# Kernel tuning notes

Hardware: AMD Instinct MI355X
Metric: run time of the kernel (lower is better)

Reference implementation:

```python
import jax, jax.numpy as jnp
import numpy as np

NUM_COMPONENTS = 4
HEADS = 16


def setup_inputs() -> dict:
    key = jax.random.key(0)
    ks = jax.random.split(key, 7)
    BC, S, D = 8, 4096, 1024      # batch_times_comp = batch(2) * num_components(4)
    Se, De = 256, 2048            # encoder seq len, encoder hidden dim
    sc = 0.02                     # keep linear outputs in a sane range
    return {
        "hidden_states": jax.random.normal(ks[0], (BC, S, D), jnp.float32),
        "encoder_hidden_states": jax.random.normal(ks[1], (BC, Se, De), jnp.float32),
        "Wq": jax.random.normal(ks[2], (D, D), jnp.float32) * sc,
        "Wk": jax.random.normal(ks[3], (De, D), jnp.float32) * sc,
        "Wv": jax.random.normal(ks[4], (De, D), jnp.float32) * sc,
        "Wo": jax.random.normal(ks[5], (D, D), jnp.float32) * sc,
        "bo": jnp.zeros((D,), jnp.float32),
    }


def reference(hidden_states, encoder_hidden_states, Wq, Wk, Wv, Wo, bo):
    C, H = NUM_COMPONENTS, HEADS
    BC, S, D = hidden_states.shape
    Se = encoder_hidden_states.shape[1]
    B = BC // C
    dh = D // H
    scale = dh ** -0.5  # attn.scale (learn_temperature=False)

    # projections -> [BC, H, S(e), dh]
    q = (hidden_states @ Wq).reshape(BC, S, H, dh).transpose(0, 2, 1, 3)
    k = (encoder_hidden_states @ Wk).reshape(BC, Se, H, dh).transpose(0, 2, 1, 3)
    v = (encoder_hidden_states @ Wv).reshape(BC, Se, H, dh).transpose(0, 2, 1, 3)

    # dense scores [BC, H, S, Se]
    scores = jnp.einsum("bhsd,bhtd->bhst", q, k) * scale
    # softmax over the COMPONENT axis (dim 0 after the 5D view)
    scores5 = scores.reshape(C, B, H, S, Se)
    w = jax.nn.softmax(scores5, axis=0)  # [C, B, H, S, Se]

    # compositional (negative) entropy, summed over components -> [B, H, S, Se]
    compositional_entropy = (w * jnp.log(w)).sum(axis=0)

    # rescale and attend
    w = (w * (C / Se)).reshape(BC, H, S, Se)
    out = jnp.einsum("bhst,bhtd->bhsd", w, v)
    out = out.transpose(0, 2, 1, 3).reshape(BC, S, D)

    # to_out[0] linear (+bias), to_out[1] dropout = identity at eval,
    # residual connection, rescale_output_factor = 1
    out = out @ Wo + bo + hidden_states
    return out, compositional_entropy
```

## Files before the change

### kernel.cpp

```cpp
#include <hip/hip_runtime.h>

typedef unsigned short u16;
typedef __bf16 bf16x4 __attribute__((ext_vector_type(4)));
typedef __bf16 bf16x8 __attribute__((ext_vector_type(8)));
typedef float f32x4 __attribute__((ext_vector_type(4)));
typedef u16 u16x4 __attribute__((ext_vector_type(4)));
typedef u16 u16x8 __attribute__((ext_vector_type(8)));

#define AS1P(p) ((__attribute__((address_space(1))) void*)(unsigned long long)(p))
#define AS3P(p) ((__attribute__((address_space(3))) void*)(unsigned long long)(p))
#define MFMA16(a, b, c) __builtin_amdgcn_mfma_f32_16x16x32_bf16((a), (b), (c), 0, 0, 0)

__device__ __forceinline__ u16 f2b(float x) { return __builtin_bit_cast(u16, (__bf16)x); }
__device__ __forceinline__ float b2f(u16 u) {
  return __builtin_bit_cast(float, (unsigned)u << 16);
}

__global__ __launch_bounds__(256) void cvt_f32_bf16(const float* __restrict__ in,
                                                    u16* __restrict__ out, int n4) {
  int stride = gridDim.x * blockDim.x;
  for (int i = blockIdx.x * blockDim.x + threadIdx.x; i < n4; i += stride) {
    f32x4 v = *(const f32x4*)(in + (long)i * 4);
    u16x4 o;
    o[0] = f2b(v[0]); o[1] = f2b(v[1]); o[2] = f2b(v[2]); o[3] = f2b(v[3]);
    *(u16x4*)(out + (long)i * 4) = o;
  }
}

__global__ __launch_bounds__(256) void wtrans(const float* __restrict__ W,
                                              u16* __restrict__ Wt, int K, int N) {
  __shared__ float tile[32][33];
  int nbk = K >> 5;
  int bk = blockIdx.x % nbk;
  int bn = blockIdx.x / nbk;
  int tx = threadIdx.x & 31, ty = threadIdx.x >> 5;
#pragma unroll
  for (int i = 0; i < 32; i += 8)
    tile[ty + i][tx] = W[(long)(bk * 32 + ty + i) * N + bn * 32 + tx];
  __syncthreads();
#pragma unroll
  for (int i = 0; i < 32; i += 8)
    Wt[(long)(bn * 32 + ty + i) * K + bk * 32 + tx] = f2b(tile[tx][ty + i]);
}

__global__ __launch_bounds__(256) void vtrans(const u16* __restrict__ kvb,
                                              u16* __restrict__ vt) {
  __shared__ u16 tile[32][33];
  int bt = blockIdx.x & 7;
  int bd = (blockIdx.x >> 3) & 31;
  int bc = blockIdx.x >> 8;
  int tx = threadIdx.x & 31, ty = threadIdx.x >> 5;
  const long ob = (long)bc * 1024 * 256;
  const float RS = 1.0f / 64.0f;
#pragma unroll
  for (int i = 0; i < 32; i += 8)
    tile[ty + i][tx] =
        kvb[((long)bc * 256 + bt * 32 + ty + i) * 2048 + 1024 + bd * 32 + tx];
  __syncthreads();
#pragma unroll
  for (int i = 0; i < 32; i += 8)
    vt[ob + (long)(bd * 32 + ty + i) * 256 + bt * 32 + tx] =
        f2b(b2f(tile[tx][ty + i]) * RS);
}

__global__ __launch_bounds__(256) void kfrag_build(const u16* __restrict__ kvb,
                                                   u16* __restrict__ kfrag) {
  int wv = ((int)blockIdx.x << 2) + (threadIdx.x >> 6);
  int lane = threadIdx.x & 63, lr = lane & 15, lg = lane >> 4;
  int ks = wv & 1, tsl = (wv >> 1) & 1, c = (wv >> 2) & 3;
  int ch = (wv >> 4) & 7, h = (wv >> 7) & 15, b = (wv >> 11) & 1;
  const u16* src = kvb + ((long)(c * 2 + b) * 256 + ch * 32 + tsl * 16 + lr) * 2048 +
                   h * 64 + ks * 32 + lg * 8;
  *(bf16x8*)(kfrag + (long)wv * 512 + lane * 8) = *(const bf16x8*)src;
}

__global__ __launch_bounds__(256) void vfrag_build(const u16* __restrict__ vtb,
                                                   u16* __restrict__ vfrag) {
  int wv = ((int)blockIdx.x << 2) + (threadIdx.x >> 6);
  int lane = threadIdx.x & 63, lr = lane & 15, lg = lane >> 4;
  int dsu = wv & 3, c = (wv >> 2) & 3;
  int ch = (wv >> 4) & 7, h = (wv >> 7) & 15, b = (wv >> 11) & 1;
  const u16* src = vtb + ((long)(c * 2 + b) * 1024 + h * 64 + dsu * 16 + lr) * 256 +
                   ch * 32 + lg * 8;
  *(bf16x8*)(vfrag + (long)wv * 512 + lane * 8) = *(const bf16x8*)src;
}

__global__ __launch_bounds__(256) void gemm_bt(
    const u16* __restrict__ A, const u16* __restrict__ Bt,
    u16* __restrict__ outb, int M, int N, int K, float ascale) {
  __shared__ u16 lA[128 * 64];
  __shared__ u16 lB[128 * 64];
  const int tid = threadIdx.x;
  const int lane = tid & 63;
  const int wid = tid >> 6;
  const int wm = wid >> 1, wn = wid & 1;
  const int lr = lane & 15, lg = lane >> 4;

  int bid = (int)blockIdx.x;
  int nwg = (int)gridDim.x;
  if ((nwg & 7) == 0) bid = (bid & 7) * (nwg >> 3) + (bid >> 3);

  const int nbn = N >> 7;
  const int bm = bid / nbn;
  const int bn = bid % nbn;
  const long arow0 = (long)bm * 128;
  const long brow0 = (long)bn * 128;

  f32x4 acc[4][4] = {};

  const int srow = tid >> 3;
  const int scol = tid & 7;

  for (int k0 = 0; k0 < K; k0 += 64) {
#pragma unroll
    for (int i = 0; i < 4; ++i) {
      int row = i * 32 + srow;
      int kc = scol ^ (row & 7);
      __builtin_amdgcn_global_load_lds(AS1P(A + (arow0 + row) * K + k0 + kc * 8),
                                       AS3P(lA + i * 2048 + (tid & ~63) * 8), 16, 0, 0);
    }
#pragma unroll
    for (int i = 0; i < 4; ++i) {
      int row = i * 32 + srow;
      int kc = scol ^ (row & 7);
      __builtin_amdgcn_global_load_lds(AS1P(Bt + (brow0 + row) * K + k0 + kc * 8),
                                       AS3P(lB + i * 2048 + (tid & ~63) * 8), 16, 0, 0);
    }
    asm volatile("s_waitcnt vmcnt(0)" ::: "memory");
    __syncthreads();

#pragma unroll
    for (int ks = 0; ks < 2; ++ks) {
      bf16x8 af[4], bfr[4];
#pragma unroll
      for (int m = 0; m < 4; ++m) {
        int row = wm * 64 + m * 16 + lr;
        int off = row * 128 + ks * 64 + lg * 16;
        off ^= (row & 7) << 4;
        af[m] = *(const bf16x8*)((const char*)lA + off);
      }
#pragma unroll
      for (int n = 0; n < 4; ++n) {
        int row = wn * 64 + n * 16 + lr;
        int off = row * 128 + ks * 64 + lg * 16;
        off ^= (row & 7) << 4;
        bfr[n] = *(const bf16x8*)((const char*)lB + off);
      }
#pragma unroll
      for (int m = 0; m < 4; ++m)
#pragma unroll
        for (int n = 0; n < 4; ++n)
          acc[m][n] = MFMA16(af[m], bfr[n], acc[m][n]);
    }
    __syncthreads();
  }

#pragma unroll
  for (int m = 0; m < 4; ++m)
#pragma unroll
    for (int n = 0; n < 4; ++n) {
      long col = brow0 + wn * 64 + n * 16 + lr;
#pragma unroll
      for (int r = 0; r < 4; ++r) {
        long row = arow0 + wm * 64 + m * 16 + lg * 4 + r;
        outb[row * N + col] = f2b(acc[m][n][r] * ascale);
      }
    }
}

template <int MODE>
__global__ __launch_bounds__(512, 2) void gemm256(
    const u16* __restrict__ A, const u16* __restrict__ Bt,
    u16* __restrict__ outb, float* __restrict__ outf,
    const float* __restrict__ bias, const u16* __restrict__ residb,
    int M, int N, int K, float ascale) {
  __shared__ u16 lds[2][2][256 * 64];
  const int tid = threadIdx.x;
  const int lane = tid & 63;
  const int wid = tid >> 6;
  const int wm = wid >> 2;
  const int wn = wid & 3;
  const int lr = lane & 15, lg = lane >> 4;

  int bid = (int)blockIdx.x;
  int nwg = (int)gridDim.x;
  bid = (bid & 7) * (nwg >> 3) + (bid >> 3);

  const int nbn = N >> 8;
  const int bm = bid / nbn;
  const int bn = bid % nbn;
  const long arow0 = (long)bm * 256;
  const long brow0 = (long)bn * 256;

  f32x4 acc[8][4] = {};

  const int srow = tid >> 3;
  const int scol = tid & 7;
  const int nt = K >> 6;

#define STAGE256(bf, t)                                                                \
  do {                                                                                 \
    int k0_ = (t) << 6;                                                                \
    _Pragma("unroll") for (int i = 0; i < 4; ++i) {                                    \
      int row = i * 64 + srow;                                                         \
      int kc = scol ^ (row & 7);                                                       \
      __builtin_amdgcn_global_load_lds(AS1P(A + (arow0 + row) * K + k0_ + kc * 8),     \
                                       AS3P(&lds[bf][0][0] + i * 4096 + (tid & ~63) * 8), \
                                       16, 0, 0);                                      \
    }                                                                                  \
    _Pragma("unroll") for (int i = 0; i < 4; ++i) {                                    \
      int row = i * 64 + srow;                                                         \
      int kc = scol ^ (row & 7);                                                       \
      __builtin_amdgcn_global_load_lds(AS1P(Bt + (brow0 + row) * K + k0_ + kc * 8),    \
                                       AS3P(&lds[bf][1][0] + i * 4096 + (tid & ~63) * 8), \
                                       16, 0, 0);                                      \
    }                                                                                  \
  } while (0)

#define COMPUTE256(bf)                                                                 \
  do {                                                                                 \
    _Pragma("unroll") for (int ks = 0; ks < 2; ++ks) {                                 \
      bf16x8 af[8], bfr[4];                                                            \
      _Pragma("unroll") for (int m = 0; m < 8; ++m) {                                  \
        int row = wm * 128 + m * 16 + lr;                                              \
        int off = row * 128 + ks * 64 + lg * 16;                                       \
        off ^= (row & 7) << 4;                                                         \
        af[m] = *(const bf16x8*)((const char*)&lds[bf][0][0] + off);                   \
      }                                                                                \
      _Pragma("unroll") for (int n = 0; n < 4; ++n) {                                  \
        int row = wn * 64 + n * 16 + lr;                                               \
        int off = row * 128 + ks * 64 + lg * 16;                                       \
        off ^= (row & 7) << 4;                                                         \
        bfr[n] = *(const bf16x8*)((const char*)&lds[bf][1][0] + off);                  \
      }                                                                                \
      _Pragma("unroll") for (int m = 0; m < 8; ++m)                                    \
          _Pragma("unroll") for (int n = 0; n < 4; ++n)                                \
              acc[m][n] = MFMA16(af[m], bfr[n], acc[m][n]);                            \
    }                                                                                  \
  } while (0)

  STAGE256(0, 0);
  asm volatile("s_waitcnt vmcnt(0)" ::: "memory");
  __syncthreads();
  int cur = 0;
  for (int t = 0; t < nt - 1; ++t) {
    STAGE256(cur ^ 1, t + 1);
    COMPUTE256(cur);
    asm volatile("s_waitcnt vmcnt(0)" ::: "memory");
    __syncthreads();
    cur ^= 1;
  }
  COMPUTE256(cur);

#pragma unroll
  for (int m = 0; m < 8; ++m)
#pragma unroll
    for (int n = 0; n < 4; ++n) {
      long col = brow0 + wn * 64 + n * 16 + lr;
#pragma unroll
      for (int r = 0; r < 4; ++r) {
        long row = arow0 + wm * 128 + m * 16 + lg * 4 + r;
        float v = acc[m][n][r];
        if (MODE == 1) {
          long idx = row * N + col;
          __builtin_nontemporal_store(v + bias[col] + b2f(residb[idx]), outf + idx);
        } else {
          outb[row * N + col] = f2b(v * ascale);
        }
      }
    }
#undef STAGE256
#undef COMPUTE256
}

__global__ __launch_bounds__(256, 1) void attn_fused(
    const u16* q,
    const u16* __restrict__ kfrag,
    const u16* __restrict__ vfrag,
    u16* attnout,
    float* __restrict__ ent) {
  const int B = 2, H = 16, S = 4096, Se = 256, D = 1024;
  __shared__ u16 kvs[2][32 * 512];
  __shared__ u16 ldsP[4 * 4608];
  const int tid = threadIdx.x;
  const int lane = tid & 63, wid = tid >> 6;
  const int lr = lane & 15, lg = lane >> 4;
  int bid = (int)blockIdx.x;
  bid = (bid & 7) * 128 + (bid >> 3);
  const int sblk = bid & 31;
  const int h = (bid >> 5) & 15;
  const int b = bid >> 9;
  const int s0 = sblk * 128 + wid * 32;

  u16* Pw = ldsP + wid * 4608;

  bf16x8 qf[4][2][2];
#pragma unroll
  for (int c = 0; c < 4; ++c)
#pragma unroll
    for (int st = 0; st < 2; ++st)
#pragma unroll
      for (int ks = 0; ks < 2; ++ks)
        qf[c][st][ks] =
            *(const bf16x8*)(q + ((c * B + b) * (long)S + s0 + st * 16 + lr) * D +
                             h * 64 + ks * 32 + lg * 8);

  const u16* kbh = kfrag + (long)(b * 16 + h) * 65536;
  const u16* vbh = vfrag + (long)(b * 16 + h) * 65536;
  float* entp = ent + ((long)(b * H + h) * S + s0 + lg * 4) * Se + lr;

  const float LN2 = 0.69314718056f;
  const int g0 = wid * 8;

  f32x4 oacc[4][4][2] = {};

#define STAGEKV(buf, ch)                                                               \
  do {                                                                                 \
    _Pragma("unroll") for (int j = 0; j < 8; ++j) {                                    \
      int f = g0 + j;                                                                  \
      const u16* src = (f < 16 ? kbh + (ch) * 8192 + f * 512                           \
                               : vbh + (ch) * 8192 + (f - 16) * 512) +                 \
                       lane * 8;                                                       \
      __builtin_amdgcn_global_load_lds(AS1P(src), AS3P(&kvs[buf][f * 512]), 16, 0, 0); \
    }                                                                                  \
  } while (0)

  STAGEKV(0, 0);
  __syncthreads();

#pragma unroll
  for (int ch = 0; ch < 8; ++ch) {
    const int cur = ch & 1;
    if (ch < 7) STAGEKV(cur ^ 1, ch + 1);
    const u16* KV = kvs[cur];

    f32x4 sacc[2][4][2] = {};
#pragma unroll
    for (int c = 0; c < 4; ++c)
#pragma unroll
      for (int tsl = 0; tsl < 2; ++tsl)
#pragma unroll
        for (int ks = 0; ks < 2; ++ks) {
          bf16x8 kfv = *(const bf16x8*)(KV + (c * 4 + tsl * 2 + ks) * 512 + lane * 8);
#pragma unroll
          for (int st = 0; st < 2; ++st)
            sacc[st][c][tsl] = MFMA16(qf[c][st][ks], kfv, sacc[st][c][tsl]);
        }

#pragma unroll
    for (int st = 0; st < 2; ++st) {
#pragma unroll
      for (int tsl = 0; tsl < 2; ++tsl) {
#pragma unroll
        for (int r = 0; r < 4; ++r) {
          float t0 = sacc[st][0][tsl][r];
          float t1 = sacc[st][1][tsl][r];
          float t2 = sacc[st][2][tsl][r];
          float t3 = sacc[st][3][tsl][r];
          float e0 = __builtin_amdgcn_exp2f(t0);
          float e1 = __builtin_amdgcn_exp2f(t1);
          float e2 = __builtin_amdgcn_exp2f(t2);
          float e3 = __builtin_amdgcn_exp2f(t3);
          float sum = (e0 + e1) + (e2 + e3);
          float inv = __builtin_amdgcn_rcpf(sum);
          float l2s = __builtin_amdgcn_logf(sum);
          float w0 = e0 * inv, w1 = e1 * inv, w2 = e2 * inv, w3 = e3 * inv;
          float entv = (w0 * t0 + w1 * t1 + w2 * t2 + w3 * t3 - l2s) * LN2;
          __builtin_nontemporal_store(
              entv, entp + (st * 16 + r) * Se + ch * 32 + tsl * 16);
          int prow = st * 16 + lg * 4 + r;
          int pof = prow * 36 + tsl * 16 + lr;
          Pw[0 * 1152 + pof] = f2b(w0);
          Pw[1 * 1152 + pof] = f2b(w1);
          Pw[2 * 1152 + pof] = f2b(w2);
          Pw[3 * 1152 + pof] = f2b(w3);
        }
      }
    }

#pragma unroll
    for (int c = 0; c < 4; ++c) {
      bf16x8 pf[2];
#pragma unroll
      for (int st = 0; st < 2; ++st) {
        union { bf16x4 hh[2]; bf16x8 v; } pu;
        pu.hh[0] = *(const bf16x4*)(Pw + c * 1152 + (st * 16 + lr) * 36 + lg * 8);
        pu.hh[1] = *(const bf16x4*)(Pw + c * 1152 + (st * 16 + lr) * 36 + lg * 8 + 4);
        pf[st] = pu.v;
      }
#pragma unroll
      for (int dsu = 0; dsu < 4; ++dsu) {
        bf16x8 vfv = *(const bf16x8*)(KV + (16 + c * 4 + dsu) * 512 + lane * 8);
        oacc[c][dsu][0] = MFMA16(pf[0], vfv, oacc[c][dsu][0]);
        oacc[c][dsu][1] = MFMA16(pf[1], vfv, oacc[c][dsu][1]);
      }
    }

    __syncthreads();
  }

#pragma unroll
  for (int c = 0; c < 4; ++c)
#pragma unroll
    for (int dsu = 0; dsu < 4; ++dsu)
#pragma unroll
      for (int st = 0; st < 2; ++st)
#pragma unroll
        for (int r = 0; r < 4; ++r) {
          long s = s0 + st * 16 + lg * 4 + r;
          attnout[((c * B + b) * (long)S + s) * D + h * 64 + dsu * 16 + lr] =
              f2b(oacc[c][dsu][st][r]);
        }
#undef STAGEKV
}

extern "C" void kernel_launch(void* const* d_in, const int* in_sizes, int n_in,
                              void* d_out, int out_size, void* d_ws, size_t ws_size,
                              hipStream_t stream) {
  const float* hs  = (const float*)d_in[0];
  const float* ehs = (const float*)d_in[1];
  const float* Wq  = (const float*)d_in[2];
  const float* Wk  = (const float*)d_in[3];
  const float* Wv  = (const float*)d_in[4];
  const float* Wo  = (const float*)d_in[5];
  const float* bo  = (const float*)d_in[6];
  float* out = (float*)d_out;
  float* ent = out + (size_t)8 * 4096 * 1024;

  char* ws = (char*)d_ws;
  u16* hsb   = (u16*)(ws);
  u16* ehsb  = (u16*)(ws + 67108864);
  u16* kfrag = (u16*)(ws + 67108864);
  u16* vfrag = (u16*)(ws + 71303168);
  u16* wqT   = (u16*)(ws + 75497472);
  u16* wkT   = (u16*)(ws + 77594624);
  u16* wvT   = (u16*)(ws + 81788928);
  u16* woT   = (u16*)(ws + 85983232);
  u16* qb    = (u16*)(ws + 88080384);
  u16* kvb   = (u16*)(ws + 155189248);
  u16* vtb   = (u16*)(ws + 163577856);

  const float QSCALE = 0.125f * 1.44269504f;

  cvt_f32_bf16<<<2048, 256, 0, stream>>>(hs, hsb, (8 * 4096 * 1024) / 4);
  cvt_f32_bf16<<<512, 256, 0, stream>>>(ehs, ehsb, (8 * 256 * 2048) / 4);
  wtrans<<<1024, 256, 0, stream>>>(Wq, wqT, 1024, 1024);
  wtrans<<<2048, 256, 0, stream>>>(Wk, wkT, 2048, 1024);
  wtrans<<<2048, 256, 0, stream>>>(Wv, wvT, 2048, 1024);
  wtrans<<<1024, 256, 0, stream>>>(Wo, woT, 1024, 1024);
  gemm256<0><<<(32768 / 256) * (1024 / 256), 512, 0, stream>>>(
      hsb, wqT, qb, nullptr, nullptr, nullptr, 32768, 1024, 1024, QSCALE);
  gemm_bt<<<(2048 / 128) * (2048 / 128), 256, 0, stream>>>(
      ehsb, wkT, kvb, 2048, 2048, 2048, 1.0f);
  vtrans<<<2048, 256, 0, stream>>>(kvb, vtb);
  kfrag_build<<<1024, 256, 0, stream>>>(kvb, kfrag);
  vfrag_build<<<1024, 256, 0, stream>>>(vtb, vfrag);
  attn_fused<<<1024, 256, 0, stream>>>(qb, kfrag, vfrag, qb, ent);
  gemm256<1><<<(32768 / 256) * (1024 / 256), 512, 0, stream>>>(
      qb, woT, nullptr, out, bo, hsb, 32768, 1024, 1024, 1.0f);
}
```

Baseline: 371.2 us.

## Split gemm256 tiles into 128-row halves with fine-grained staged load/MFMA pipeline

Restructures the 256x256 GEMM mainloop so that A and B tiles are staged in 128-row halves, with each half-tile global->LDS load issued between quadrant MFMA phases. The aim is to overlap memory traffic with compute at finer granularity, in the style of a ping-pong schedule. It uses vmcnt(4) partial waits, s_setprio around the MFMA blocks and sched_barriers. The per-wave output mapping changes to 2x2 quadrants of 64x32. This adds many barriers per K-step, and the partial waitcnt and LDS buffer-reuse logic need to be right for correctness.

```diff
diff --git a/kernel.cpp b/kernel.cpp
--- a/kernel.cpp
+++ b/kernel.cpp
@@ -174,7 +174,7 @@
     u16* __restrict__ outb, float* __restrict__ outf,
     const float* __restrict__ bias, const u16* __restrict__ residb,
     int M, int N, int K, float ascale) {
-  __shared__ u16 lds[2][2][256 * 64];
+  __shared__ u16 lds[2][2][2][128 * 64];
   const int tid = threadIdx.x;
   const int lane = tid & 63;
   const int wid = tid >> 6;
@@ -198,79 +198,136 @@
   const int scol = tid & 7;
   const int nt = K >> 6;
 
-#define STAGE256(bf, t)                                                                \
+#define STAGE_REG(srcp, rbase, dstp, hf, t)                                            \
   do {                                                                                 \
     int k0_ = (t) << 6;                                                                \
-    _Pragma("unroll") for (int i = 0; i < 4; ++i) {                                    \
-      int row = i * 64 + srow;                                                         \
+    _Pragma("unroll") for (int i = 0; i < 2; ++i) {                                    \
+      int row = (hf) * 128 + i * 64 + srow;                                            \
       int kc = scol ^ (row & 7);                                                       \
-      __builtin_amdgcn_global_load_lds(AS1P(A + (arow0 + row) * K + k0_ + kc * 8),     \
-                                       AS3P(&lds[bf][0][0] + i * 4096 + (tid & ~63) * 8), \
-                                       16, 0, 0);                                      \
-    }                                                                                  \
-    _Pragma("unroll") for (int i = 0; i < 4; ++i) {                                    \
-      int row = i * 64 + srow;                                                         \
-      int kc = scol ^ (row & 7);                                                       \
-      __builtin_amdgcn_global_load_lds(AS1P(Bt + (brow0 + row) * K + k0_ + kc * 8),    \
-                                       AS3P(&lds[bf][1][0] + i * 4096 + (tid & ~63) * 8), \
-                                       16, 0, 0);                                      \
+      __builtin_amdgcn_global_load_lds(                                                \
+          AS1P((srcp) + (long)((rbase) + row) * K + k0_ + kc * 8),                     \
+          AS3P((dstp) + i * 4096 + (tid & ~63) * 8), 16, 0, 0);                        \
     }                                                                                  \
   } while (0)
 
-#define COMPUTE256(bf)                                                                 \
+#define READ_AF(b, mh)                                                                 \
   do {                                                                                 \
-    _Pragma("unroll") for (int ks = 0; ks < 2; ++ks) {                                 \
-      bf16x8 af[8], bfr[4];                                                            \
-      _Pragma("unroll") for (int m = 0; m < 8; ++m) {                                  \
-        int row = wm * 128 + m * 16 + lr;                                              \
-        int off = row * 128 + ks * 64 + lg * 16;                                       \
-        off ^= (row & 7) << 4;                                                         \
-        af[m] = *(const bf16x8*)((const char*)&lds[bf][0][0] + off);                   \
-      }                                                                                \
-      _Pragma("unroll") for (int n = 0; n < 4; ++n) {                                  \
-        int row = wn * 64 + n * 16 + lr;                                               \
-        int off = row * 128 + ks * 64 + lg * 16;                                       \
-        off ^= (row & 7) << 4;                                                         \
-        bfr[n] = *(const bf16x8*)((const char*)&lds[bf][1][0] + off);                  \
-      }                                                                                \
-      _Pragma("unroll") for (int m = 0; m < 8; ++m)                                    \
-          _Pragma("unroll") for (int n = 0; n < 4; ++n)                                \
-              acc[m][n] = MFMA16(af[m], bfr[n], acc[m][n]);                            \
+    _Pragma("unroll") for (int mm = 0; mm < 4; ++mm)                                   \
+        _Pragma("unroll") for (int ks = 0; ks < 2; ++ks) {                             \
+      int rl = wm * 64 + mm * 16 + lr;                                                 \
+      int off = rl * 128 + ks * 64 + lg * 16;                                          \
+      off ^= (rl & 7) << 4;                                                            \
+      af[mm][ks] = *(const bf16x8*)((const char*)&lds[b][mh][0][0] + off);             \
     }                                                                                  \
   } while (0)
 
-  STAGE256(0, 0);
-  asm volatile("s_waitcnt vmcnt(0)" ::: "memory");
-  __syncthreads();
-  int cur = 0;
-  for (int t = 0; t < nt - 1; ++t) {
-    STAGE256(cur ^ 1, t + 1);
-    COMPUTE256(cur);
-    asm volatile("s_waitcnt vmcnt(0)" ::: "memory");
-    __syncthreads();
-    cur ^= 1;
+#define READ_BF(b, nh, dst)                                                            \
+  do {                                                                                 \
+    _Pragma("unroll") for (int nn = 0; nn < 2; ++nn)                                   \
+        _Pragma("unroll") for (int ks = 0; ks < 2; ++ks) {                             \
+      int rl = wn * 32 + nn * 16 + lr;                                                 \
+      int off = rl * 128 + ks * 64 + lg * 16;                                          \
+      off ^= (rl & 7) << 4;                                                            \
+      dst[nn][ks] = *(const bf16x8*)((const char*)&lds[b][nh][1][0] + off);            \
+    }                                                                                  \
+  } while (0)
+
+#define DO_MFMA(mh, nh, bfr)                                                           \
+  do {                                                                                 \
+    __builtin_amdgcn_s_setprio(1);                                                     \
+    _Pragma("unroll") for (int mm = 0; mm < 4; ++mm)                                   \
+        _Pragma("unroll") for (int nn = 0; nn < 2; ++nn)                               \
+            _Pragma("unroll") for (int ks = 0; ks < 2; ++ks)                           \
+                acc[(mh) * 4 + mm][(nh) * 2 + nn] = MFMA16(                            \
+                    af[mm][ks], bfr[nn][ks], acc[(mh) * 4 + mm][(nh) * 2 + nn]);       \
+    __builtin_amdgcn_s_setprio(0);                                                     \
+  } while (0)
+
+#define WAIT4()  asm volatile("s_waitcnt vmcnt(4)" ::: "memory")
+#define WAIT0()  asm volatile("s_waitcnt vmcnt(0)" ::: "memory")
+#define LGKM0()  asm volatile("s_waitcnt lgkmcnt(0)" ::: "memory")
+#define BAR()    __builtin_amdgcn_s_barrier()
+#define SCHED0() __builtin_amdgcn_sched_barrier(0)
+
+  STAGE_REG(A,  arow0, &lds[0][0][0][0], 0, 0);
+  STAGE_REG(Bt, brow0, &lds[0][0][1][0], 0, 0);
+  STAGE_REG(Bt, brow0, &lds[0][1][1][0], 1, 0);
+  STAGE_REG(A,  arow0, &lds[0][1][0][0], 1, 0);
+  WAIT4();
+  BAR();
+  SCHED0();
+
+  for (int T = 0; T < nt; ++T) {
+    const int b = T & 1;
+    const bool last = (T == nt - 1);
+    bf16x8 af[4][2], bf0[2][2], bf1[2][2];
+    READ_AF(b, 0);
+    READ_BF(b, 0, bf0);
+    if (!last) {
+      STAGE_REG(A, arow0, &lds[b ^ 1][0][0][0], 0, T + 1);
+      WAIT4();
+    } else {
+      WAIT0();
+    }
+    BAR(); LGKM0(); SCHED0();
+    DO_MFMA(0, 0, bf0);
+    BAR(); SCHED0();
+    READ_BF(b, 1, bf1);
+    if (!last) {
+      STAGE_REG(Bt, brow0, &lds[b ^ 1][0][1][0], 0, T + 1);
+      WAIT4();
+    }
+    BAR(); LGKM0(); SCHED0();
+    DO_MFMA(0, 1, bf1);
+    BAR(); SCHED0();
+    READ_AF(b, 1);
+    if (!last) {
+      STAGE_REG(Bt, brow0, &lds[b ^ 1][1][1][0], 1, T + 1);
+      WAIT4();
+    }
+    BAR(); LGKM0(); SCHED0();
+    DO_MFMA(1, 0, bf0);
+    BAR(); SCHED0();
+    if (!last) {
+      STAGE_REG(A, arow0, &lds[b ^ 1][1][0][0], 1, T + 1);
+      WAIT4();
+    }
+    BAR(); SCHED0();
+    DO_MFMA(1, 1, bf1);
+    BAR(); SCHED0();
   }
-  COMPUTE256(cur);
-
-#pragma unroll
-  for (int m = 0; m < 8; ++m)
-#pragma unroll
-    for (int n = 0; n < 4; ++n) {
-      long col = brow0 + wn * 64 + n * 16 + lr;
-#pragma unroll
-      for (int r = 0; r < 4; ++r) {
-        long row = arow0 + wm * 128 + m * 16 + lg * 4 + r;
-        float v = acc[m][n][r];
-        if (MODE == 1) {
-          long idx = row * N + col;
-          __builtin_nontemporal_store(v + bias[col] + b2f(residb[idx]), outf + idx);
-        } else {
-          outb[row * N + col] = f2b(v * ascale);
+
+#pragma unroll
+  for (int mh = 0; mh < 2; ++mh)
+#pragma unroll
+    for (int mm = 0; mm < 4; ++mm)
+#pragma unroll
+      for (int nh = 0; nh < 2; ++nh)
+#pragma unroll
+        for (int nn = 0; nn < 2; ++nn) {
+          long col = brow0 + nh * 128 + wn * 32 + nn * 16 + lr;
+#pragma unroll
+          for (int r = 0; r < 4; ++r) {
+            long row = arow0 + mh * 128 + wm * 64 + mm * 16 + lg * 4 + r;
+            float v = acc[mh * 4 + mm][nh * 2 + nn][r];
+            if (MODE == 1) {
+              long idx = row * N + col;
+              __builtin_nontemporal_store(v + bias[col] + b2f(residb[idx]),
+                                          outf + idx);
+            } else {
+              outb[row * N + col] = f2b(v * ascale);
+            }
+          }
         }
-      }
-    }
-#undef STAGE256
-#undef COMPUTE256
+#undef STAGE_REG
+#undef READ_AF
+#undef READ_BF
+#undef DO_MFMA
+#undef WAIT4
+#undef WAIT0
+#undef LGKM0
+#undef BAR
+#undef SCHED0
 }
 
 __global__ __launch_bounds__(256, 1) void attn_fused(
```

Result: no change. 374.8 us (+1.0%).
